# Kernel optimization log

Measured on AMD Instinct MI355X. Metric: run time of the kernel, lower is better.

## Reference

```python
import jax, jax.numpy as jnp
import numpy as np

THETA = 10.0      # spike threshold
TAU_SR = 1.0      # SRM (psp) kernel time constant
TAU_REF = 1.0     # refractory kernel time constant
SCALE_REF = 2.0   # refractory kernel scale (SLAYER default: -2*theta peak)


@jax.custom_vjp
def spike_fn(v):
    # Heaviside on (membrane - theta); surrogate gradient in bwd (SLAYER-style pdf)
    return (v >= 0.0).astype(v.dtype)

def _spike_fwd(v):
    return spike_fn(v), v

def _spike_bwd(v, g):
    return (g * jnp.exp(-jnp.abs(v) / THETA) / THETA,)

spike_fn.defvjp(_spike_fwd, _spike_bwd)


def alpha_psp(x, tau):
    """Causal conv of x (T, B, F) with alpha kernel eps[k] = (k/tau)*exp(1-k/tau),
    implemented as a 2-state linear recurrence (exact for the discrete kernel)."""
    d = jnp.float32(np.exp(-1.0 / tau))
    c = jnp.float32(np.e / tau)

    def step(carry, xt):
        p, q = carry
        q = d * (q + p)          # q[t] = sum_s x[s]*(t-s)*d^(t-s)
        p = d * p + xt           # p[t] = sum_s x[s]*d^(t-s)
        return (p, q), c * q

    z = jnp.zeros_like(x[0])
    _, out = jax.lax.scan(step, (z, z), x)
    return out


def spike_dyn(u, tau_ref, scale_ref, theta):
    """Threshold-with-refractory dynamics. u: (T, B, F) synaptic drive.
    membrane[t] = u[t] - scale_ref*theta * (alpha refractory conv of past spikes)."""
    d = jnp.float32(np.exp(-1.0 / tau_ref))
    c = jnp.float32(np.e / tau_ref)
    cref = jnp.float32(-scale_ref * theta) * c

    def step(carry, ut):
        p, q = carry
        q = d * (q + p)                       # refractory trace (lag-0 coeff is 0)
        s = spike_fn(ut + cref * q - theta)   # spike if membrane >= theta
        p = d * p + s
        return (p, q), s

    z = jnp.zeros_like(u[0])
    _, s = jax.lax.scan(step, (z, z), u)
    return s


def setup_inputs() -> dict:
    key = jax.random.key(0)
    k1, k2, k3 = jax.random.split(key, 3)
    # sparse binary input spike trains, (B, C, H, W, T) SLAYER layout
    downsampled = (jax.random.uniform(k1, (16, 2, 50, 63, 500)) < 0.1).astype(jnp.float32)
    w1 = jax.random.normal(k2, (1024, 6300), dtype=jnp.float32) * 0.1
    w2 = jax.random.normal(k3, (20, 1024), dtype=jnp.float32) * 0.1
    return {"downsampled": downsampled, "w1": w1, "w2": w2}


def reference(downsampled, w1, w2):
    B, T = downsampled.shape[0], downsampled.shape[-1]
    x = downsampled.reshape(B, -1, T).transpose(2, 0, 1)   # (T, B, 6300)
    p1 = alpha_psp(x, TAU_SR)                              # psp filter
    u1 = jnp.einsum('tbf,of->tbo', p1, w1)                 # fc1 (per-timestep dense)
    s1 = spike_dyn(u1, TAU_REF, SCALE_REF, THETA)          # spike layer 1
    p2 = alpha_psp(s1, TAU_SR)
    u2 = jnp.einsum('tbh,oh->tbo', p2, w2)                 # fc2
    s2 = spike_dyn(u2, TAU_REF, SCALE_REF, THETA)
    return s2.transpose(1, 2, 0)                           # (B, output_size, T)
```

## Files before the change

### kernel.cpp

```cpp
#include <hip/hip_runtime.h>
#include <cstdint>
#include <cstddef>

#define T_N   500
#define B_N   16
#define F_IN  6300
#define KW    198
#define KPAD  6336
#define H1    1024
#define H2    20
#define N2P   32
#define M_N   8000
#define M_PADN 8064

#define DD_C   0.36787944117144233f
#define CC_C   2.718281828459045f
#define THETA_C 10.0f
#define INV2048 4.8828125e-4f

typedef _Float16 half8 __attribute__((ext_vector_type(8)));
typedef __attribute__((ext_vector_type(4))) float f32x4;

__device__ __forceinline__ unsigned short f2h_bits(float x) {
    union { _Float16 h; unsigned short u; } c; c.h = (_Float16)x; return c.u;
}
__device__ __forceinline__ float h2f(unsigned short u) {
    union { _Float16 h; unsigned short u; } c; c.u = u; return (float)c.h;
}

__global__ void prep_bits_t_k(const float* __restrict__ in, uint32_t* __restrict__ bits_t) {
    const int tch = blockIdx.x;
    const int w   = blockIdx.y;
    const int b   = blockIdx.z;
    const int t   = tch * 64 + threadIdx.x;
    if (t >= 504) return;
    const int m = t * 16 + b;
    uint32_t word = 0u;
    if (t < T_N) {
        const int fbase = w * 32;
        #pragma unroll
        for (int j = 0; j < 32; ++j) {
            const int f = fbase + j;
            float v = 0.f;
            if (f < F_IN) v = in[((size_t)b * F_IN + f) * T_N + t];
            word |= (v != 0.f ? 1u : 0u) << j;
        }
    }
    bits_t[(size_t)w * M_PADN + m] = word;
}

__global__ void split2_w1_k(const float* __restrict__ w1, unsigned short* __restrict__ w1f) {
    const int o = blockIdx.y;
    const int f = blockIdx.x * 256 + threadIdx.x;
    if (f >= KPAD) return;
    float w = (f < F_IN) ? w1[(size_t)o * F_IN + f] : 0.f;
    const unsigned short h1 = f2h_bits(w);
    const float r1 = w - h2f(h1);
    const unsigned short h2 = f2h_bits(r1 * 2048.0f);
    const size_t base = (size_t)o * KPAD + f;
    w1f[base]                      = h1;
    w1f[(size_t)H1 * KPAD + base]  = h2;
}

__global__ void split2_w2_k(const float* __restrict__ w2, unsigned short* __restrict__ w2f) {
    const int o = blockIdx.y;
    const int k = blockIdx.x * 256 + threadIdx.x;
    float w = (o < H2) ? w2[(size_t)o * H1 + k] : 0.f;
    const unsigned short h1 = f2h_bits(w);
    const float r1 = w - h2f(h1);
    const unsigned short h2 = f2h_bits(r1 * 2048.0f);
    const size_t base = (size_t)o * H1 + k;
    w2f[base]                      = h1;
    w2f[(size_t)N2P * H1 + base]   = h2;
}

__global__ __launch_bounds__(256, 2)
void gemm1_mfma_k(const uint32_t* __restrict__ bits_t,
                  const unsigned short* __restrict__ w1f,
                  float* __restrict__ u1) {
    __shared__ uint32_t AsU[128 * 16];
    __shared__ uint32_t BsU[2 * 128 * 16];

    const int tid  = threadIdx.x;
    const int lane = tid & 63;
    const int wave = tid >> 6;
    const int wr = wave >> 1, wc = wave & 1;
    const int n0 = blockIdx.x * 128;
    const int m0 = blockIdx.y * 128;
    const int l15 = lane & 15, g = lane >> 4;

    const unsigned short* bsrc0 =
        w1f + (size_t)(n0 + (lane >> 2)) * KPAD + (lane & 3) * 8;

    const int arow_w = tid & 127;
    const int ah     = tid >> 7;
    const int axor   = (arow_w >> 1) & 3;
    const int apos0  = (2 * ah) ^ axor;
    const int apos1  = (2 * ah + 1) ^ axor;

    f32x4 acc[2][4][4];
    const f32x4 fz = {0.f, 0.f, 0.f, 0.f};
    #pragma unroll
    for (int t = 0; t < 2; ++t)
        #pragma unroll
        for (int i = 0; i < 4; ++i)
            #pragma unroll
            for (int j = 0; j < 4; ++j) acc[t][i][j] = fz;

    int aoff[4], boff[4];
    #pragma unroll
    for (int mi = 0; mi < 4; ++mi) {
        const int ar = wr * 64 + mi * 16 + l15;
        aoff[mi] = ar * 16 + ((g ^ ((ar >> 1) & 3)) << 2);
    }
    #pragma unroll
    for (int ni = 0; ni < 4; ++ni) {
        const int br = wc * 64 + ni * 16 + l15;
        boff[ni] = br * 16 + (g << 2);
    }

    for (int kw = 0; kw < KW; ++kw) {
        __syncthreads();
        #pragma unroll
        for (int j = 0; j < 4; ++j) {
            const int e    = wave * 4 + j;
            const int term = e >> 3;
            const int ii   = e & 7;
            const unsigned short* src =
                bsrc0 + (size_t)(term * H1 + ii * 16) * KPAD + kw * 32;
            __builtin_amdgcn_global_load_lds(
                (const __attribute__((address_space(1))) uint32_t*)src,
                (__attribute__((address_space(3))) uint32_t*)&BsU[term * 2048 + ii * 256],
                16, 0, 0);
        }
        {
            const uint32_t word = bits_t[(size_t)kw * M_PADN + m0 + arow_w];
            uint32_t v[8];
            #pragma unroll
            for (int i = 0; i < 8; ++i) {
                const int b0 = ah * 16 + 2 * i;
                v[i] = (((word >> b0) & 1u) ? 0x00003C00u : 0u) |
                       (((word >> (b0 + 1)) & 1u) ? 0x3C000000u : 0u);
            }
            *(uint4*)&AsU[arow_w * 16 + apos0 * 4] = make_uint4(v[0], v[1], v[2], v[3]);
            *(uint4*)&AsU[arow_w * 16 + apos1 * 4] = make_uint4(v[4], v[5], v[6], v[7]);
        }
        __syncthreads();

        half8 af[4];
        #pragma unroll
        for (int mi = 0; mi < 4; ++mi) af[mi] = *(const half8*)&AsU[aoff[mi]];
        #pragma unroll
        for (int term = 0; term < 2; ++term) {
            half8 bfv[4];
            #pragma unroll
            for (int ni = 0; ni < 4; ++ni)
                bfv[ni] = *(const half8*)&BsU[term * 2048 + boff[ni]];
            #pragma unroll
            for (int mi = 0; mi < 4; ++mi)
                #pragma unroll
                for (int ni = 0; ni < 4; ++ni)
                    acc[term][mi][ni] = __builtin_amdgcn_mfma_f32_16x16x32_f16(
                        af[mi], bfv[ni], acc[term][mi][ni], 0, 0, 0);
        }
    }

    #pragma unroll
    for (int mi = 0; mi < 4; ++mi) {
        const int mbase = m0 + wr * 64 + mi * 16 + g * 4;
        #pragma unroll
        for (int ni = 0; ni < 4; ++ni) {
            const int o = n0 + wc * 64 + ni * 16 + l15;
            #pragma unroll
            for (int r = 0; r < 4; ++r)
                u1[(size_t)(mbase + r) * H1 + o] =
                    acc[0][mi][ni][r] + acc[1][mi][ni][r] * INV2048;
        }
    }
}

__global__ void scan1_k(const float* __restrict__ u1, unsigned short* __restrict__ s1f) {
    const int lane = blockIdx.x * 64 + threadIdx.x;
    const float CREF = -20.0f * CC_C;
    float p1 = 0.f, q1 = 0.f, pr = 0.f, qr = 0.f;
    float A[10], Bv[10];

#define STEP1(xv, tidx) {                                   \
        q1 = DD_C * (q1 + p1); p1 = DD_C * p1 + (xv);       \
        const float uu = CC_C * q1;                         \
        qr = DD_C * (qr + pr);                              \
        const float vv = uu + CREF * qr - THETA_C;          \
        const float ss = (vv >= 0.f) ? 1.f : 0.f;           \
        pr = DD_C * pr + ss;                                \
        s1f[(size_t)(tidx) * 16384 + lane] =                \
            (vv >= 0.f) ? (unsigned short)0x3C00 : (unsigned short)0; }

    #pragma unroll
    for (int j = 0; j < 10; ++j) A[j] = u1[(size_t)j * 16384 + lane];
    for (int it = 0; it < 25; ++it) {
        const int gB = 2 * it + 1;
        #pragma unroll
        for (int j = 0; j < 10; ++j) Bv[j] = u1[(size_t)(gB * 10 + j) * 16384 + lane];
        #pragma unroll
        for (int j = 0; j < 10; ++j) STEP1(A[j], (2 * it) * 10 + j);
        if (it < 24) {
            const int gA = 2 * it + 2;
            #pragma unroll
            for (int j = 0; j < 10; ++j) A[j] = u1[(size_t)(gA * 10 + j) * 16384 + lane];
        }
        #pragma unroll
        for (int j = 0; j < 10; ++j) STEP1(Bv[j], gB * 10 + j);
    }
#undef STEP1
}

__global__ __launch_bounds__(256)
void gemm2_mfma_k(const unsigned short* __restrict__ s1f,
                  const unsigned short* __restrict__ w2f,
                  float* __restrict__ u2) {
    __shared__ uint32_t AsU[128 * 16];
    __shared__ uint32_t BsU[2 * 32 * 16];

    const int tid  = threadIdx.x;
    const int lane = tid & 63;
    const int wave = tid >> 6;
    const int m0 = blockIdx.x * 128;
    const int l15 = lane & 15, g = lane >> 4;

    f32x4 acc[2][2][2];
    const f32x4 fz = {0.f, 0.f, 0.f, 0.f};
    #pragma unroll
    for (int t = 0; t < 2; ++t)
        #pragma unroll
        for (int i = 0; i < 2; ++i)
            #pragma unroll
            for (int j = 0; j < 2; ++j) acc[t][i][j] = fz;

    int aoff[2], boff[2][2];
    #pragma unroll
    for (int mi = 0; mi < 2; ++mi) {
        const int ar = wave * 32 + mi * 16 + l15;
        aoff[mi] = ar * 16 + ((g ^ ((ar >> 1) & 3)) << 2);
    }
    #pragma unroll
    for (int term = 0; term < 2; ++term)
        #pragma unroll
        for (int ni = 0; ni < 2; ++ni) {
            const int br = ni * 16 + l15;
            boff[term][ni] = term * 512 + br * 16 + ((g ^ ((br >> 1) & 3)) << 2);
        }

    for (int kw = 0; kw < 32; ++kw) {
        __syncthreads();
        #pragma unroll
        for (int i = 0; i < 2; ++i) {
            const int c   = i * 256 + tid;
            const int row = c >> 2;
            const int kc  = c & 3;
            const unsigned short* src =
                s1f + (size_t)(m0 + row) * H1 + kw * 32 + (kc ^ ((row >> 1) & 3)) * 8;
            __builtin_amdgcn_global_load_lds(
                (const __attribute__((address_space(1))) uint32_t*)src,
                (__attribute__((address_space(3))) uint32_t*)&AsU[(i * 256 + wave * 64) * 4],
                16, 0, 0);
        }
        {
            const int c    = tid;
            const int term = c >> 7;
            const int o    = (c >> 2) & 31;
            const int kc   = c & 3;
            const unsigned short* src =
                w2f + (size_t)(term * N2P + o) * H1 + kw * 32 + (kc ^ ((o >> 1) & 3)) * 8;
            __builtin_amdgcn_global_load_lds(
                (const __attribute__((address_space(1))) uint32_t*)src,
                (__attribute__((address_space(3))) uint32_t*)&BsU[wave * 256],
                16, 0, 0);
        }
        __syncthreads();

        half8 af[2];
        #pragma unroll
        for (int mi = 0; mi < 2; ++mi) af[mi] = *(const half8*)&AsU[aoff[mi]];
        #pragma unroll
        for (int term = 0; term < 2; ++term)
            #pragma unroll
            for (int ni = 0; ni < 2; ++ni) {
                const half8 bf = *(const half8*)&BsU[boff[term][ni]];
                #pragma unroll
                for (int mi = 0; mi < 2; ++mi)
                    acc[term][mi][ni] = __builtin_amdgcn_mfma_f32_16x16x32_f16(
                        af[mi], bf, acc[term][mi][ni], 0, 0, 0);
            }
    }

    #pragma unroll
    for (int mi = 0; mi < 2; ++mi) {
        const int mbase = m0 + wave * 32 + mi * 16 + g * 4;
        #pragma unroll
        for (int ni = 0; ni < 2; ++ni) {
            const int o = ni * 16 + l15;
            if (o < H2) {
                #pragma unroll
                for (int r = 0; r < 4; ++r)
                    u2[(size_t)(mbase + r) * H2 + o] =
                        acc[0][mi][ni][r] + acc[1][mi][ni][r] * INV2048;
            }
        }
    }
}

__global__ void scan2_k(const float* __restrict__ u2, float* __restrict__ out) {
    const int lane = blockIdx.x * 64 + threadIdx.x;
    if (lane >= 320) return;
    const float CREF = -20.0f * CC_C;
    float p1 = 0.f, q1 = 0.f, pr = 0.f, qr = 0.f;
    float A[10], Bv[10];

#define STEP2(xv, tidx) {                                   \
        q1 = DD_C * (q1 + p1); p1 = DD_C * p1 + (xv);       \
        const float uu = CC_C * q1;                         \
        qr = DD_C * (qr + pr);                              \
        const float vv = uu + CREF * qr - THETA_C;          \
        const float ss = (vv >= 0.f) ? 1.f : 0.f;           \
        pr = DD_C * pr + ss;                                \
        out[(size_t)lane * T_N + (tidx)] = ss; }

    #pragma unroll
    for (int j = 0; j < 10; ++j) A[j] = u2[(size_t)j * 320 + lane];
    for (int it = 0; it < 25; ++it) {
        const int gB = 2 * it + 1;
        #pragma unroll
        for (int j = 0; j < 10; ++j) Bv[j] = u2[(size_t)(gB * 10 + j) * 320 + lane];
        #pragma unroll
        for (int j = 0; j < 10; ++j) STEP2(A[j], (2 * it) * 10 + j);
        if (it < 24) {
            const int gA = 2 * it + 2;
            #pragma unroll
            for (int j = 0; j < 10; ++j) A[j] = u2[(size_t)(gA * 10 + j) * 320 + lane];
        }
        #pragma unroll
        for (int j = 0; j < 10; ++j) STEP2(Bv[j], gB * 10 + j);
    }
#undef STEP2
}

extern "C" void kernel_launch(void* const* d_in, const int* in_sizes, int n_in,
                              void* d_out, int out_size, void* d_ws, size_t ws_size,
                              hipStream_t stream) {
    const float* x  = (const float*)d_in[0];
    const float* w1 = (const float*)d_in[1];
    const float* w2 = (const float*)d_in[2];
    float* out = (float*)d_out;

    char* ws = (char*)d_ws;
    size_t off = 0;
    uint32_t*       bits_t = (uint32_t*)(ws + off);       off += (size_t)KW * M_PADN * 4;
    unsigned short* w1f    = (unsigned short*)(ws + off); off += (size_t)2 * H1 * KPAD * 2;
    unsigned short* w2f    = (unsigned short*)(ws + off); off += (size_t)2 * N2P * H1 * 2;
    float*          u1     = (float*)(ws + off);          off += (size_t)M_PADN * H1 * 4;
    unsigned short* s1f    = (unsigned short*)(ws + off); off += (size_t)M_PADN * H1 * 2;
    float*          u2     = (float*)(ws + off);          off += (size_t)M_PADN * H2 * 4;
    (void)ws_size; (void)in_sizes; (void)n_in; (void)out_size;

    prep_bits_t_k <<<dim3(8, KW, B_N), 64,  0, stream>>>(x, bits_t);
    split2_w1_k   <<<dim3(25, H1),     256, 0, stream>>>(w1, w1f);
    split2_w2_k   <<<dim3(4, N2P),     256, 0, stream>>>(w2, w2f);
    gemm1_mfma_k  <<<dim3(8, 63),      256, 0, stream>>>(bits_t, w1f, u1);
    scan1_k       <<<256,              64,  0, stream>>>(u1, s1f);
    gemm2_mfma_k  <<<63,               256, 0, stream>>>(s1f, w2f, u2);
    scan2_k       <<<5,                64,  0, stream>>>(u2, out);
}
```

Measured before the change: 353.5 us.

## Double-buffer gemm1 smem, split gemm2 over K, and fuse prep kernels

Fuses the three preprocessing kernels into one launch with 256-thread blocks. Gemm1 now uses double-buffered LDS so the next tile's global-to-LDS loads and A-unpack overlap the current MFMA work, with one barrier per step and raised wave priority around the MFMAs. Gemm2 is split four ways along K to get more blocks, writing partial sums that scan2 adds on load. The trade-offs are doubled LDS use in gemm1 and extra partial-sum traffic in scan2.

```diff
diff --git a/kernel.cpp b/kernel.cpp
--- a/kernel.cpp
+++ b/kernel.cpp
@@ -28,58 +28,69 @@
     union { _Float16 h; unsigned short u; } c; c.u = u; return (float)c.h;
 }
 
-__global__ void prep_bits_t_k(const float* __restrict__ in, uint32_t* __restrict__ bits_t) {
-    const int tch = blockIdx.x;
-    const int w   = blockIdx.y;
-    const int b   = blockIdx.z;
-    const int t   = tch * 64 + threadIdx.x;
-    if (t >= 504) return;
-    const int m = t * 16 + b;
-    uint32_t word = 0u;
-    if (t < T_N) {
-        const int fbase = w * 32;
-        #pragma unroll
-        for (int j = 0; j < 32; ++j) {
-            const int f = fbase + j;
-            float v = 0.f;
-            if (f < F_IN) v = in[((size_t)b * F_IN + f) * T_N + t];
-            word |= (v != 0.f ? 1u : 0u) << j;
-        }
-    }
-    bits_t[(size_t)w * M_PADN + m] = word;
-}
-
-__global__ void split2_w1_k(const float* __restrict__ w1, unsigned short* __restrict__ w1f) {
-    const int o = blockIdx.y;
-    const int f = blockIdx.x * 256 + threadIdx.x;
-    if (f >= KPAD) return;
-    float w = (f < F_IN) ? w1[(size_t)o * F_IN + f] : 0.f;
-    const unsigned short h1 = f2h_bits(w);
-    const float r1 = w - h2f(h1);
-    const unsigned short h2 = f2h_bits(r1 * 2048.0f);
-    const size_t base = (size_t)o * KPAD + f;
-    w1f[base]                      = h1;
-    w1f[(size_t)H1 * KPAD + base]  = h2;
-}
-
-__global__ void split2_w2_k(const float* __restrict__ w2, unsigned short* __restrict__ w2f) {
-    const int o = blockIdx.y;
-    const int k = blockIdx.x * 256 + threadIdx.x;
-    float w = (o < H2) ? w2[(size_t)o * H1 + k] : 0.f;
-    const unsigned short h1 = f2h_bits(w);
-    const float r1 = w - h2f(h1);
-    const unsigned short h2 = f2h_bits(r1 * 2048.0f);
-    const size_t base = (size_t)o * H1 + k;
-    w2f[base]                      = h1;
-    w2f[(size_t)N2P * H1 + base]   = h2;
+__global__ void prep_fused_k(const float* __restrict__ x,
+                             const float* __restrict__ w1,
+                             const float* __restrict__ w2,
+                             uint32_t* __restrict__ bits_t,
+                             unsigned short* __restrict__ w1f,
+                             unsigned short* __restrict__ w2f) {
+    const int bid = blockIdx.x;
+    if (bid < 6336) {
+        const int b    = bid & 15;
+        const int tmp  = bid >> 4;
+        const int w    = tmp % 198;
+        const int tch2 = tmp / 198;
+        const int t    = tch2 * 256 + threadIdx.x;
+        if (t >= 504) return;
+        const int m = t * 16 + b;
+        uint32_t word = 0u;
+        if (t < T_N) {
+            const int fbase = w * 32;
+            #pragma unroll
+            for (int j = 0; j < 32; ++j) {
+                const int f = fbase + j;
+                float v = 0.f;
+                if (f < F_IN) v = x[((size_t)b * F_IN + f) * T_N + t];
+                word |= (v != 0.f ? 1u : 0u) << j;
+            }
+        }
+        bits_t[(size_t)w * M_PADN + m] = word;
+    } else if (bid < 6336 + 1024) {
+        const int o = bid - 6336;
+        #pragma unroll 1
+        for (int it = 0; it < 25; ++it) {
+            const int f = it * 256 + threadIdx.x;
+            if (f >= KPAD) break;
+            float w = (f < F_IN) ? w1[(size_t)o * F_IN + f] : 0.f;
+            const unsigned short h1 = f2h_bits(w);
+            const float r1 = w - h2f(h1);
+            const unsigned short h2 = f2h_bits(r1 * 2048.0f);
+            const size_t base = (size_t)o * KPAD + f;
+            w1f[base]                     = h1;
+            w1f[(size_t)H1 * KPAD + base] = h2;
+        }
+    } else {
+        const int o = bid - 7360;
+        #pragma unroll
+        for (int it = 0; it < 4; ++it) {
+            const int k = it * 256 + threadIdx.x;
+            float w = (o < H2) ? w2[(size_t)o * H1 + k] : 0.f;
+            const unsigned short h1 = f2h_bits(w);
+            const float r1 = w - h2f(h1);
+            const unsigned short h2 = f2h_bits(r1 * 2048.0f);
+            const size_t base = (size_t)o * H1 + k;
+            w2f[base]                    = h1;
+            w2f[(size_t)N2P * H1 + base] = h2;
+        }
+    }
 }
 
 __global__ __launch_bounds__(256, 2)
 void gemm1_mfma_k(const uint32_t* __restrict__ bits_t,
                   const unsigned short* __restrict__ w1f,
                   float* __restrict__ u1) {
-    __shared__ uint32_t AsU[128 * 16];
-    __shared__ uint32_t BsU[2 * 128 * 16];
+    __shared__ uint32_t AsU[2][128 * 16];
+    __shared__ uint32_t BsU[2][2 * 128 * 16];
 
     const int tid  = threadIdx.x;
     const int lane = tid & 63;
@@ -119,51 +130,85 @@
         boff[ni] = br * 16 + (g << 2);
     }
 
-    for (int kw = 0; kw < KW; ++kw) {
-        __syncthreads();
-        #pragma unroll
-        for (int j = 0; j < 4; ++j) {
-            const int e    = wave * 4 + j;
-            const int term = e >> 3;
-            const int ii   = e & 7;
-            const unsigned short* src =
-                bsrc0 + (size_t)(term * H1 + ii * 16) * KPAD + kw * 32;
-            __builtin_amdgcn_global_load_lds(
-                (const __attribute__((address_space(1))) uint32_t*)src,
-                (__attribute__((address_space(3))) uint32_t*)&BsU[term * 2048 + ii * 256],
-                16, 0, 0);
-        }
-        {
-            const uint32_t word = bits_t[(size_t)kw * M_PADN + m0 + arow_w];
-            uint32_t v[8];
-            #pragma unroll
-            for (int i = 0; i < 8; ++i) {
-                const int b0 = ah * 16 + 2 * i;
-                v[i] = (((word >> b0) & 1u) ? 0x00003C00u : 0u) |
-                       (((word >> (b0 + 1)) & 1u) ? 0x3C000000u : 0u);
-            }
-            *(uint4*)&AsU[arow_w * 16 + apos0 * 4] = make_uint4(v[0], v[1], v[2], v[3]);
-            *(uint4*)&AsU[arow_w * 16 + apos1 * 4] = make_uint4(v[4], v[5], v[6], v[7]);
-        }
-        __syncthreads();
-
-        half8 af[4];
-        #pragma unroll
-        for (int mi = 0; mi < 4; ++mi) af[mi] = *(const half8*)&AsU[aoff[mi]];
-        #pragma unroll
-        for (int term = 0; term < 2; ++term) {
-            half8 bfv[4];
-            #pragma unroll
-            for (int ni = 0; ni < 4; ++ni)
-                bfv[ni] = *(const half8*)&BsU[term * 2048 + boff[ni]];
-            #pragma unroll
-            for (int mi = 0; mi < 4; ++mi)
-                #pragma unroll
-                for (int ni = 0; ni < 4; ++ni)
-                    acc[term][mi][ni] = __builtin_amdgcn_mfma_f32_16x16x32_f16(
-                        af[mi], bfv[ni], acc[term][mi][ni], 0, 0, 0);
-        }
-    }
+#define STAGE_B(tt, bb)                                                        \
+    {                                                                          \
+        _Pragma("unroll")                                                      \
+        for (int j = 0; j < 4; ++j) {                                          \
+            const int e    = wave * 4 + j;                                     \
+            const int term = e >> 3;                                           \
+            const int ii   = e & 7;                                            \
+            const unsigned short* src =                                        \
+                bsrc0 + (size_t)(term * H1 + ii * 16) * KPAD + (size_t)(tt) * 32; \
+            __builtin_amdgcn_global_load_lds(                                  \
+                (const __attribute__((address_space(1))) uint32_t*)src,        \
+                (__attribute__((address_space(3))) uint32_t*)&BsU[bb][term * 2048 + ii * 256], \
+                16, 0, 0);                                                     \
+        }                                                                      \
+    }
+
+#define UNPACK_A(wrd, bb)                                                      \
+    {                                                                          \
+        uint32_t v[8];                                                         \
+        _Pragma("unroll")                                                      \
+        for (int i = 0; i < 8; ++i) {                                          \
+            const int b0 = ah * 16 + 2 * i;                                    \
+            v[i] = ((((wrd) >> b0) & 1u) ? 0x00003C00u : 0u) |                 \
+                   ((((wrd) >> (b0 + 1)) & 1u) ? 0x3C000000u : 0u);            \
+        }                                                                      \
+        *(uint4*)&AsU[bb][arow_w * 16 + apos0 * 4] = make_uint4(v[0], v[1], v[2], v[3]); \
+        *(uint4*)&AsU[bb][arow_w * 16 + apos1 * 4] = make_uint4(v[4], v[5], v[6], v[7]); \
+    }
+
+#define COMPUTE(bb)                                                            \
+    {                                                                          \
+        half8 af[4];                                                           \
+        _Pragma("unroll")                                                      \
+        for (int mi = 0; mi < 4; ++mi) af[mi] = *(const half8*)&AsU[bb][aoff[mi]]; \
+        __builtin_amdgcn_s_setprio(1);                                         \
+        _Pragma("unroll")                                                      \
+        for (int term = 0; term < 2; ++term) {                                 \
+            half8 bfv[4];                                                      \
+            _Pragma("unroll")                                                  \
+            for (int ni = 0; ni < 4; ++ni)                                     \
+                bfv[ni] = *(const half8*)&BsU[bb][term * 2048 + boff[ni]];     \
+            _Pragma("unroll")                                                  \
+            for (int mi = 0; mi < 4; ++mi)                                     \
+                _Pragma("unroll")                                              \
+                for (int ni = 0; ni < 4; ++ni)                                 \
+                    acc[term][mi][ni] = __builtin_amdgcn_mfma_f32_16x16x32_f16( \
+                        af[mi], bfv[ni], acc[term][mi][ni], 0, 0, 0);          \
+        }                                                                      \
+        __builtin_amdgcn_s_setprio(0);                                         \
+    }
+
+#define ITER(tt, curbb)                                                        \
+    {                                                                          \
+        const uint32_t wnext =                                                 \
+            bits_t[(size_t)((tt) + 1) * M_PADN + m0 + arow_w];                 \
+        STAGE_B((tt) + 1, (curbb) ^ 1);                                        \
+        COMPUTE(curbb);                                                        \
+        UNPACK_A(wnext, (curbb) ^ 1);                                          \
+        __syncthreads();                                                       \
+    }
+
+    {
+        const uint32_t w0 = bits_t[(size_t)0 * M_PADN + m0 + arow_w];
+        STAGE_B(0, 0);
+        UNPACK_A(w0, 0);
+    }
+    __syncthreads();
+
+    for (int t = 0; t < KW - 2; t += 2) {
+        ITER(t, 0);
+        ITER(t + 1, 1);
+    }
+    ITER(KW - 2, 0);
+    COMPUTE(1);
+
+#undef ITER
+#undef COMPUTE
+#undef UNPACK_A
+#undef STAGE_B
 
     #pragma unroll
     for (int mi = 0; mi < 4; ++mi) {
@@ -217,7 +262,7 @@
 __global__ __launch_bounds__(256)
 void gemm2_mfma_k(const unsigned short* __restrict__ s1f,
                   const unsigned short* __restrict__ w2f,
-                  float* __restrict__ u2) {
+                  float* __restrict__ u2p) {
     __shared__ uint32_t AsU[128 * 16];
     __shared__ uint32_t BsU[2 * 32 * 16];
 
@@ -225,6 +270,7 @@
     const int lane = tid & 63;
     const int wave = tid >> 6;
     const int m0 = blockIdx.x * 128;
+    const int kc = blockIdx.y;
     const int l15 = lane & 15, g = lane >> 4;
 
     f32x4 acc[2][2][2];
@@ -250,15 +296,16 @@
             boff[term][ni] = term * 512 + br * 16 + ((g ^ ((br >> 1) & 3)) << 2);
         }
 
-    for (int kw = 0; kw < 32; ++kw) {
+    for (int kw8 = 0; kw8 < 8; ++kw8) {
+        const int kw = kc * 8 + kw8;
         __syncthreads();
         #pragma unroll
         for (int i = 0; i < 2; ++i) {
             const int c   = i * 256 + tid;
             const int row = c >> 2;
-            const int kc  = c & 3;
+            const int kch = c & 3;
             const unsigned short* src =
-                s1f + (size_t)(m0 + row) * H1 + kw * 32 + (kc ^ ((row >> 1) & 3)) * 8;
+                s1f + (size_t)(m0 + row) * H1 + kw * 32 + (kch ^ ((row >> 1) & 3)) * 8;
             __builtin_amdgcn_global_load_lds(
                 (const __attribute__((address_space(1))) uint32_t*)src,
                 (__attribute__((address_space(3))) uint32_t*)&AsU[(i * 256 + wave * 64) * 4],
@@ -268,9 +315,9 @@
             const int c    = tid;
             const int term = c >> 7;
             const int o    = (c >> 2) & 31;
-            const int kc   = c & 3;
+            const int kch  = c & 3;
             const unsigned short* src =
-                w2f + (size_t)(term * N2P + o) * H1 + kw * 32 + (kc ^ ((o >> 1) & 3)) * 8;
+                w2f + (size_t)(term * N2P + o) * H1 + kw * 32 + (kch ^ ((o >> 1) & 3)) * 8;
             __builtin_amdgcn_global_load_lds(
                 (const __attribute__((address_space(1))) uint32_t*)src,
                 (__attribute__((address_space(3))) uint32_t*)&BsU[wave * 256],
@@ -299,22 +346,29 @@
         #pragma unroll
         for (int ni = 0; ni < 2; ++ni) {
             const int o = ni * 16 + l15;
-            if (o < H2) {
-                #pragma unroll
-                for (int r = 0; r < 4; ++r)
-                    u2[(size_t)(mbase + r) * H2 + o] =
-                        acc[0][mi][ni][r] + acc[1][mi][ni][r] * INV2048;
-            }
-        }
-    }
-}
-
-__global__ void scan2_k(const float* __restrict__ u2, float* __restrict__ out) {
+            #pragma unroll
+            for (int r = 0; r < 4; ++r)
+                u2p[((size_t)kc * M_PADN + mbase + r) * N2P + o] =
+                    acc[0][mi][ni][r] + acc[1][mi][ni][r] * INV2048;
+        }
+    }
+}
+
+__global__ void scan2_k(const float* __restrict__ u2p, float* __restrict__ out) {
     const int lane = blockIdx.x * 64 + threadIdx.x;
     if (lane >= 320) return;
+    const int b  = lane / 20;
+    const int o2 = lane % 20;
+    const int boffs = b * N2P + o2;
     const float CREF = -20.0f * CC_C;
     float p1 = 0.f, q1 = 0.f, pr = 0.f, qr = 0.f;
     float A[10], Bv[10];
+
+#define LOAD2(tidx)                                                         \
+    (u2p[(size_t)0 * M_PADN * N2P + (size_t)(tidx) * 512 + boffs] +         \
+     u2p[(size_t)1 * M_PADN * N2P + (size_t)(tidx) * 512 + boffs] +         \
+     u2p[(size_t)2 * M_PADN * N2P + (size_t)(tidx) * 512 + boffs] +         \
+     u2p[(size_t)3 * M_PADN * N2P + (size_t)(tidx) * 512 + boffs])
 
 #define STEP2(xv, tidx) {                                   \
         q1 = DD_C * (q1 + p1); p1 = DD_C * p1 + (xv);       \
@@ -326,22 +380,23 @@
         out[(size_t)lane * T_N + (tidx)] = ss; }
 
     #pragma unroll
-    for (int j = 0; j < 10; ++j) A[j] = u2[(size_t)j * 320 + lane];
+    for (int j = 0; j < 10; ++j) A[j] = LOAD2(j);
     for (int it = 0; it < 25; ++it) {
         const int gB = 2 * it + 1;
         #pragma unroll
-        for (int j = 0; j < 10; ++j) Bv[j] = u2[(size_t)(gB * 10 + j) * 320 + lane];
+        for (int j = 0; j < 10; ++j) Bv[j] = LOAD2(gB * 10 + j);
         #pragma unroll
         for (int j = 0; j < 10; ++j) STEP2(A[j], (2 * it) * 10 + j);
         if (it < 24) {
             const int gA = 2 * it + 2;
             #pragma unroll
-            for (int j = 0; j < 10; ++j) A[j] = u2[(size_t)(gA * 10 + j) * 320 + lane];
+            for (int j = 0; j < 10; ++j) A[j] = LOAD2(gA * 10 + j);
         }
         #pragma unroll
         for (int j = 0; j < 10; ++j) STEP2(Bv[j], gB * 10 + j);
     }
 #undef STEP2
+#undef LOAD2
 }
 
 extern "C" void kernel_launch(void* const* d_in, const int* in_sizes, int n_in,
@@ -359,14 +414,12 @@
     unsigned short* w2f    = (unsigned short*)(ws + off); off += (size_t)2 * N2P * H1 * 2;
     float*          u1     = (float*)(ws + off);          off += (size_t)M_PADN * H1 * 4;
     unsigned short* s1f    = (unsigned short*)(ws + off); off += (size_t)M_PADN * H1 * 2;
-    float*          u2     = (float*)(ws + off);          off += (size_t)M_PADN * H2 * 4;
+    float*          u2p    = (float*)(ws + off);          off += (size_t)4 * M_PADN * N2P * 4;
     (void)ws_size; (void)in_sizes; (void)n_in; (void)out_size;
 
-    prep_bits_t_k <<<dim3(8, KW, B_N), 64,  0, stream>>>(x, bits_t);
-    split2_w1_k   <<<dim3(25, H1),     256, 0, stream>>>(w1, w1f);
-    split2_w2_k   <<<dim3(4, N2P),     256, 0, stream>>>(w2, w2f);
-    gemm1_mfma_k  <<<dim3(8, 63),      256, 0, stream>>>(bits_t, w1f, u1);
-    scan1_k       <<<256,              64,  0, stream>>>(u1, s1f);
-    gemm2_mfma_k  <<<63,               256, 0, stream>>>(s1f, w2f, u2);
-    scan2_k       <<<5,                64,  0, stream>>>(u2, out);
-}
+    prep_fused_k  <<<7392,        256, 0, stream>>>(x, w1, w2, bits_t, w1f, w2f);
+    gemm1_mfma_k  <<<dim3(8, 63), 256, 0, stream>>>(bits_t, w1f, u1);
+    scan1_k       <<<256,         64,  0, stream>>>(u1, s1f);
+    gemm2_mfma_k  <<<dim3(63, 4), 256, 0, stream>>>(s1f, w2f, u2p);
+    scan2_k       <<<5,           64,  0, stream>>>(u2p, out);
+}
```

New measurement: 358.3 us. Within noise of the previous version (+1.3%).
